# Kernel tuning notes

Hardware: AMD Instinct MI355X
Metric: run time of the kernel (lower is better)

## Reference

```python
import jax, jax.numpy as jnp
import numpy as np

K = 1024          # num_embeddings
D = 256           # embedding_dim
COMMIT = 0.25
DECAY = 0.99
EPS = 1e-05


def setup_inputs() -> dict:
    key = jax.random.key(0)
    k1, k2 = jax.random.split(key)
    inputs = jax.random.normal(k1, (16, 4096, D), dtype=jnp.float32)
    weight = jax.random.normal(k2, (K, D), dtype=jnp.float32) * 0.1
    ema_cluster_size = jnp.zeros((K,), dtype=jnp.float32)
    ema_embedding_avg = weight  # initialized as a clone of the weights
    return {
        "inputs": inputs,
        "weight": weight,
        "ema_cluster_size": ema_cluster_size,
        "ema_embedding_avg": ema_embedding_avg,
    }


def reference(inputs, weight, ema_cluster_size, ema_embedding_avg):
    B = inputs.shape[0]
    flat = inputs.reshape(-1, D)                      # [N, D]
    dist = (
        jnp.sum(flat * flat, axis=1, keepdims=True)
        + jnp.sum(weight * weight, axis=1)
        - 2.0 * (flat @ weight.T)
    )                                                 # [N, K]
    idx = jnp.argmin(dist, axis=1)                    # [N] int
    # one-hot @ weight == gather
    quantized = weight[idx].reshape(inputs.shape)

    # --- EMA codebook update (training-mode side effects, returned as outputs) ---
    counts = jax.ops.segment_sum(jnp.ones_like(idx, dtype=jnp.float32), idx, num_segments=K)
    emb_sum = jax.ops.segment_sum(flat, idx, num_segments=K)  # one_hot.T @ flat
    new_cluster_size = DECAY * ema_cluster_size + (1.0 - DECAY) * counts
    new_embedding_avg = DECAY * ema_embedding_avg + (1.0 - DECAY) * emb_sum
    n = jnp.sum(new_cluster_size)
    cs = (new_cluster_size + EPS) / (n + K * EPS) * n
    new_weight = new_embedding_avg / cs[:, None]

    # --- losses + straight-through estimator ---
    e_latent_loss = jnp.mean((jax.lax.stop_gradient(quantized) - inputs) ** 2)
    q_latent_loss = jnp.mean((quantized - jax.lax.stop_gradient(inputs)) ** 2)
    vq_loss = q_latent_loss + COMMIT * e_latent_loss
    quantized_st = inputs + jax.lax.stop_gradient(quantized - inputs)

    return (
        quantized_st,
        vq_loss,
        idx.reshape(B, -1),
        new_weight,
        new_cluster_size,
        new_embedding_avg,
    )
```

## Files before the change

kernel.cpp:

```cpp
#include <hip/hip_runtime.h>

#define KC 1024
#define DD 256
#define NROWS 65536
#define BM 128
#define NT 512
#define RESCUE_EPS 0.02f
#define RB 8

typedef _Float16 f16x8 __attribute__((ext_vector_type(8)));
typedef float f32x4 __attribute__((ext_vector_type(4)));
typedef const __attribute__((address_space(1))) unsigned int* gptr_t;
typedef __attribute__((address_space(3))) unsigned int* lptr_t;

__global__ void wprep(const float* __restrict__ W, _Float16* __restrict__ wh,
                      float* __restrict__ se) {
    int k = blockIdx.x, lane = threadIdx.x;
    float4 v = reinterpret_cast<const float4*>(W + (size_t)k * DD)[lane];
    float vv[4] = {v.x, v.y, v.z, v.w};
    _Float16 h4[4];
    double s = 0.0;
#pragma unroll
    for (int q = 0; q < 4; ++q) {
        h4[q] = (_Float16)vv[q];
        s += (double)vv[q] * vv[q];
    }
    *reinterpret_cast<uint2*>(wh + (size_t)k * DD + lane * 4) = *reinterpret_cast<uint2*>(h4);
    for (int m = 32; m >= 1; m >>= 1) s += __shfl_xor(s, m, 64);
    if (lane == 0) se[k] = (float)s;
}

__global__ __launch_bounds__(256) void wtrans4(const float* __restrict__ W,
                                               float4* __restrict__ WT4) {
    __shared__ __align__(16) float4 tile[64][65];
    const int c0 = blockIdx.x * 64;
    const int t = threadIdx.x;
    for (int it = 0; it < 16; ++it) {
        int idx = it * 256 + t;
        int cl = idx >> 6, d4 = idx & 63;
        tile[cl][d4] = reinterpret_cast<const float4*>(W + (size_t)(c0 + cl) * DD)[d4];
    }
    __syncthreads();
    for (int it = 0; it < 16; ++it) {
        int idx = it * 256 + t;
        int d4 = idx >> 6, cl = idx & 63;
        WT4[(size_t)d4 * KC + c0 + cl] = tile[cl][d4];
    }
}

__global__ __launch_bounds__(NT, 2) void vq_mfma(
    const float* __restrict__ X,
    const _Float16* __restrict__ wh,
    const float* __restrict__ se,
    float* __restrict__ out_q, float* __restrict__ out_idx,
    int* __restrict__ idx_int, float* __restrict__ sx_out,
    int* __restrict__ flags, int* __restrict__ count,
    float* __restrict__ counts, double* __restrict__ loss_acc)
{
    __shared__ __align__(16) _Float16 wt[2][64 * 256];
    __shared__ float sxs[BM];
    __shared__ float ses[KC];
    __shared__ int argidx[BM];
    __shared__ double lred[8];

    const int tid = threadIdx.x;
    const int row0 = blockIdx.x * BM;
    const int w = tid >> 6, lane = tid & 63;
    const int m = lane & 15, g = lane >> 4;

    for (int i = tid; i < KC; i += NT) ses[i] = se[i];

    f16x8 ahr[8];
    {
        const float* xr = X + (size_t)(row0 + w * 16 + m) * DD;
        float p0 = 0.f, p1 = 0.f, p2 = 0.f, p3 = 0.f;
#pragma unroll
        for (int ks = 0; ks < 8; ++ks) {
            float4 a = *reinterpret_cast<const float4*>(xr + ks * 32 + g * 8);
            float4 b = *reinterpret_cast<const float4*>(xr + ks * 32 + g * 8 + 4);
            float v[8] = {a.x, a.y, a.z, a.w, b.x, b.y, b.z, b.w};
            f16x8 h;
#pragma unroll
            for (int q = 0; q < 8; ++q) h[q] = (_Float16)v[q];
            ahr[ks] = h;
            p0 = fmaf(v[0], v[0], fmaf(v[4], v[4], p0));
            p1 = fmaf(v[1], v[1], fmaf(v[5], v[5], p1));
            p2 = fmaf(v[2], v[2], fmaf(v[6], v[6], p2));
            p3 = fmaf(v[3], v[3], fmaf(v[7], v[7], p3));
        }
        float ss = (p0 + p1) + (p2 + p3);
        ss += __shfl_xor(ss, 16, 64);
        ss += __shfl_xor(ss, 32, 64);
        if (g == 0) sxs[w * 16 + m] = ss;
    }

    auto stage = [&](int ct, int buf) {
        const int base = ct * 64;
#pragma unroll
        for (int p = 0; p < 4; ++p) {
            int gi = p * NT + tid;
            int code = gi >> 5, j = gi & 31;
            int kq = j ^ (code & 31);
            const _Float16* src = wh + (size_t)(base + code) * DD + kq * 8;
            __builtin_amdgcn_global_load_lds((gptr_t)(const void*)src,
                                             (lptr_t)(void*)&wt[buf][gi * 8], 16, 0, 0);
        }
    };

    stage(0, 0);
    __syncthreads();

    float b1[4], b2[4];
    int i1[4];
#pragma unroll
    for (int j = 0; j < 4; ++j) { b1[j] = 3.4e38f; b2[j] = 3.4e38f; i1[j] = 0; }

    float sxr[4];
#pragma unroll
    for (int j = 0; j < 4; ++j) sxr[j] = sxs[w * 16 + g * 4 + j];

    for (int ct = 0; ct < 16; ++ct) {
        const int buf = ct & 1;
        if (ct < 15) stage(ct + 1, buf ^ 1);

        const _Float16* wtb = wt[buf];
        f32x4 acc[4];
#pragma unroll
        for (int cs = 0; cs < 4; ++cs) acc[cs] = (f32x4){0.f, 0.f, 0.f, 0.f};

#pragma unroll
        for (int ks = 0; ks < 8; ++ks) {
            const int kq = ks * 4 + g;
#pragma unroll
            for (int cs = 0; cs < 4; ++cs) {
                const int code = cs * 16 + m;
                const int L = code * 32 + (kq ^ (code & 31));
                f16x8 bh = *reinterpret_cast<const f16x8*>(wtb + L * 8);
                acc[cs] = __builtin_amdgcn_mfma_f32_16x16x32_f16(ahr[ks], bh, acc[cs], 0, 0, 0);
            }
        }
#pragma unroll
        for (int cs = 0; cs < 4; ++cs) {
            const int code = ct * 64 + cs * 16 + m;
            const float sec = ses[code];
#pragma unroll
            for (int j = 0; j < 4; ++j) {
                float s = __fsub_rn(__fadd_rn(sxr[j], sec), __fmul_rn(2.0f, acc[cs][j]));
                if (s < b1[j]) { b2[j] = b1[j]; b1[j] = s; i1[j] = code; }
                else if (s < b2[j]) { b2[j] = s; }
            }
        }
        __syncthreads();
    }

#pragma unroll
    for (int j = 0; j < 4; ++j) {
        float v1 = b1[j], v2 = b2[j];
        int ix = i1[j];
        for (int mm = 1; mm < 16; mm <<= 1) {
            float ov1 = __shfl_xor(v1, mm, 64);
            int oi = __shfl_xor(ix, mm, 64);
            float ov2 = __shfl_xor(v2, mm, 64);
            float nv2 = fminf(fminf(v2, ov2), fmaxf(v1, ov1));
            if (ov1 < v1 || (ov1 == v1 && oi < ix)) { v1 = ov1; ix = oi; }
            v2 = nv2;
        }
        if (m == 0) {
            int rl = w * 16 + g * 4 + j;
            argidx[rl] = ix;
            if (v2 - v1 < RESCUE_EPS) {
                int p = atomicAdd(count, 1);
                flags[p] = row0 + rl;
            }
        }
    }
    __syncthreads();

    if (tid < BM) {
        int row = row0 + tid;
        int k = argidx[tid];
        idx_int[row] = k;
        out_idx[row] = (float)k;
        sx_out[row] = sxs[tid];
        atomicAdd(&counts[k], 1.0f);
    }

    {
        double lacc = 0.0;
        const int rl = w * 16 + m;
        const int row = row0 + rl;
        const int k = argidx[rl];
        const _Float16* qh = wh + (size_t)k * DD;
        float* orow = out_q + (size_t)row * DD;
#pragma unroll
        for (int ks = 0; ks < 8; ++ks) {
            const int col = ks * 32 + g * 8;
            union { uint4 u; _Float16 h[8]; } qv, xv;
            qv.u = *reinterpret_cast<const uint4*>(qh + col);
            xv.u = *reinterpret_cast<uint4*>(&ahr[ks]);
            float o8[8];
#pragma unroll
            for (int q = 0; q < 8; ++q) {
                float xf = (float)xv.h[q];
                float qf = (float)qv.h[q];
                float df = qf - xf;
                o8[q] = xf + df;
                lacc += (double)df * df;
            }
            *reinterpret_cast<float4*>(orow + col)     = *reinterpret_cast<float4*>(&o8[0]);
            *reinterpret_cast<float4*>(orow + col + 4) = *reinterpret_cast<float4*>(&o8[4]);
        }
        for (int mm = 32; mm >= 1; mm >>= 1) lacc += __shfl_xor(lacc, mm, 64);
        if (lane == 0) lred[w] = lacc;
    }
    __syncthreads();
    if (tid == 0) {
        double t = 0.0;
        for (int i = 0; i < 8; ++i) t += lred[i];
        atomicAdd(loss_acc, t);
    }
}

__global__ __launch_bounds__(256) void rescue(
    const float* __restrict__ X, const float4* __restrict__ WT4,
    const float* __restrict__ Wf,
    const float* __restrict__ se, const float* __restrict__ sx,
    const int* __restrict__ flags, const int* __restrict__ count,
    int* __restrict__ idx_int, float* __restrict__ out_idx,
    float* __restrict__ out_q, float* __restrict__ counts,
    double* __restrict__ loss_acc)
{
    __shared__ __align__(16) float xs[RB][DD];
    __shared__ float rv[RB][256];
    __shared__ int ri[RB][256];
    __shared__ float sxr_s[RB];
    __shared__ int rows_s[RB];
    __shared__ int kn_s[RB], ko_s[RB];
    __shared__ double dred[4];
    const int t = threadIdx.x;
    const int n = count[0];

    for (int base = blockIdx.x * RB; base < n; base += gridDim.x * RB) {
        const int nb = min(RB, n - base);
        for (int idx = t; idx < nb * 64; idx += 256) {
            int r = idx >> 6, c4 = idx & 63;
            float4 v = reinterpret_cast<const float4*>(X + (size_t)flags[base + r] * DD)[c4];
            *reinterpret_cast<float4*>(&xs[r][c4 * 4]) = v;
        }
        if (t < nb) { rows_s[t] = flags[base + t]; sxr_s[t] = sx[flags[base + t]]; }
        __syncthreads();

        float acc[4][RB];
#pragma unroll
        for (int cc = 0; cc < 4; ++cc)
#pragma unroll
            for (int r = 0; r < RB; ++r) acc[cc][r] = 0.0f;

        float4 wv[4], wn[4];
#pragma unroll
        for (int cc = 0; cc < 4; ++cc) wv[cc] = WT4[(size_t)0 * KC + cc * 256 + t];

        for (int d4 = 0; d4 < 64; ++d4) {
            const int dn = (d4 < 63) ? d4 + 1 : 63;
#pragma unroll
            for (int cc = 0; cc < 4; ++cc) wn[cc] = WT4[(size_t)dn * KC + cc * 256 + t];
#pragma unroll
            for (int r = 0; r < RB; ++r) {
                float4 xv = *reinterpret_cast<const float4*>(&xs[r][d4 * 4]);
#pragma unroll
                for (int cc = 0; cc < 4; ++cc)
                    acc[cc][r] = fmaf(xv.w, wv[cc].w, fmaf(xv.z, wv[cc].z,
                                 fmaf(xv.y, wv[cc].y, fmaf(xv.x, wv[cc].x, acc[cc][r]))));
            }
#pragma unroll
            for (int cc = 0; cc < 4; ++cc) wv[cc] = wn[cc];
        }

        float best[RB];
        int bidx[RB];
#pragma unroll
        for (int r = 0; r < RB; ++r) { best[r] = 3.4e38f; bidx[r] = 0; }
#pragma unroll
        for (int cc = 0; cc < 4; ++cc) {
            const int c = cc * 256 + t;
            const float sec = se[c];
#pragma unroll
            for (int r = 0; r < RB; ++r) {
                float s = __fsub_rn(__fadd_rn(sxr_s[r], sec), __fmul_rn(2.0f, acc[cc][r]));
                if (s < best[r] || (s == best[r] && c < bidx[r])) { best[r] = s; bidx[r] = c; }
            }
        }
#pragma unroll
        for (int r = 0; r < RB; ++r) { rv[r][t] = best[r]; ri[r][t] = bidx[r]; }
        __syncthreads();

        for (int sft = 128; sft >= 1; sft >>= 1) {
            if (t < sft) {
#pragma unroll
                for (int r = 0; r < RB; ++r) {
                    float ov = rv[r][t + sft];
                    int oi = ri[r][t + sft];
                    if (ov < rv[r][t] || (ov == rv[r][t] && oi < ri[r][t])) {
                        rv[r][t] = ov; ri[r][t] = oi;
                    }
                }
            }
            __syncthreads();
        }
        if (t < nb) {
            int row = rows_s[t];
            int kn = ri[t][0], ko = idx_int[row];
            kn_s[t] = kn; ko_s[t] = ko;
            if (kn != ko) {
                idx_int[row] = kn;
                out_idx[row] = (float)kn;
                atomicAdd(&counts[ko], -1.0f);
                atomicAdd(&counts[kn], 1.0f);
            }
        }
        __syncthreads();

        for (int r = 0; r < nb; ++r) {
            const int ko = ko_s[r], kn = kn_s[r];
            if (kn != ko) {
                const int row = rows_s[r];
                float x = xs[r][t];
                float qo = Wf[(size_t)ko * DD + t];
                float qn = Wf[(size_t)kn * DD + t];
                float dfn = qn - x, dfo = qo - x;
                out_q[(size_t)row * DD + t] = x + dfn;
                double dl = (double)dfn * dfn - (double)dfo * dfo;
                for (int mm = 32; mm >= 1; mm >>= 1) dl += __shfl_xor(dl, mm, 64);
                if ((t & 63) == 0) dred[t >> 6] = dl;
                __syncthreads();
                if (t == 0) atomicAdd(loss_acc, dred[0] + dred[1] + dred[2] + dred[3]);
                __syncthreads();
            }
        }
        __syncthreads();
    }
}

__global__ void prefix1024(const float* __restrict__ counts, int* __restrict__ off,
                           int* __restrict__ cur) {
    __shared__ int s[1024];
    int t = threadIdx.x;
    s[t] = (int)counts[t];
    __syncthreads();
    for (int d = 1; d < 1024; d <<= 1) {
        int v = (t >= d) ? s[t - d] : 0;
        __syncthreads();
        s[t] += v;
        __syncthreads();
    }
    off[t] = (t == 0) ? 0 : s[t - 1];
    cur[t] = 0;
    if (t == 0) off[1024] = 65536;
}

__global__ __launch_bounds__(256) void scatter_rows(
    const int* __restrict__ idx_int, const int* __restrict__ off,
    int* __restrict__ cur, int* __restrict__ sorted) {
    int i = blockIdx.x * 256 + threadIdx.x;
    int k = idx_int[i];
    int p = atomicAdd(&cur[k], 1);
    sorted[off[k] + p] = i;
}

__global__ __launch_bounds__(256) void emb_gather(
    const float* __restrict__ X, const int* __restrict__ off,
    const int* __restrict__ sorted, float* __restrict__ emb) {
    const int k = blockIdx.x, t = threadIdx.x;
    const int s0 = off[k], s1 = off[k + 1];
    float a0 = 0.f, a1 = 0.f, a2 = 0.f, a3 = 0.f;
    int i = s0;
    for (; i + 4 <= s1; i += 4) {
        int r0 = sorted[i], r1 = sorted[i + 1], r2 = sorted[i + 2], r3 = sorted[i + 3];
        a0 += X[(size_t)r0 * DD + t];
        a1 += X[(size_t)r1 * DD + t];
        a2 += X[(size_t)r2 * DD + t];
        a3 += X[(size_t)r3 * DD + t];
    }
    for (; i < s1; ++i) a0 += X[(size_t)sorted[i] * DD + t];
    emb[(size_t)k * DD + t] = (a0 + a1) + (a2 + a3);
}

__global__ void fin1(const float* __restrict__ ema_cs, float* __restrict__ ncs_buf,
                     const double* __restrict__ loss_acc, float* __restrict__ out_loss,
                     float* __restrict__ n_out)
{
    __shared__ float red[1024];
    int t = threadIdx.x;
    const float OM = (float)(1.0 - 0.99);
    float ncs = __fadd_rn(__fmul_rn(0.99f, ema_cs[t]), __fmul_rn(OM, ncs_buf[t]));
    ncs_buf[t] = ncs;
    red[t] = ncs;
    __syncthreads();
    for (int s = 512; s >= 1; s >>= 1) {
        if (t < s) red[t] += red[t + s];
        __syncthreads();
    }
    if (t == 0) {
        n_out[0] = red[0];
        float el = (float)(loss_acc[0] / 16777216.0);
        out_loss[0] = __fadd_rn(el, __fmul_rn(0.25f, el));
    }
}

__global__ __launch_bounds__(256) void fin2(const float* __restrict__ ema_avg,
                                            float* __restrict__ avg_buf,
                                            const float* __restrict__ ncs,
                                            const float* __restrict__ n_ptr,
                                            float* __restrict__ out_w)
{
    int k = blockIdx.x, d = threadIdx.x;
    const float OM = (float)(1.0 - 0.99);
    const float KEPS = (float)(1024.0 * 1e-5);
    size_t i = (size_t)k * DD + d;
    float avg = __fadd_rn(__fmul_rn(0.99f, ema_avg[i]), __fmul_rn(OM, avg_buf[i]));
    float n = n_ptr[0];
    float cs = __fmul_rn(__fdiv_rn(__fadd_rn(ncs[k], 1e-5f), __fadd_rn(n, KEPS)), n);
    avg_buf[i] = avg;
    out_w[i] = __fdiv_rn(avg, cs);
}

extern "C" void kernel_launch(void* const* d_in, const int* in_sizes, int n_in,
                              void* d_out, int out_size, void* d_ws, size_t ws_size,
                              hipStream_t stream) {
    const float* X = (const float*)d_in[0];
    const float* W = (const float*)d_in[1];
    const float* ema_cs = (const float*)d_in[2];
    const float* ema_avg = (const float*)d_in[3];

    float* out = (float*)d_out;
    float* out_q    = out;
    float* out_loss = out + 16777216;
    float* out_idx  = out + 16777217;
    float* out_w    = out + 16842753;
    float* out_ncs  = out + 17104897;
    float* out_avg  = out + 17105921;

    char* ws = (char*)d_ws;
    float* se      = (float*)(ws + 0);
    float* n_ptr   = (float*)(ws + 4096);
    double* loss   = (double*)(ws + 4112);
    int*   count   = (int*)(ws + 4128);
    _Float16* wh   = (_Float16*)(ws + 8192);
    float* sx      = (float*)(ws + 1056768);
    int*   idx_int = (int*)(ws + 1318912);
    int*   flags   = (int*)(ws + 1581056);
    float4* WT4    = (float4*)(ws + 2097152);
    int*   off     = (int*)(ws + 3145728);
    int*   cur     = (int*)(ws + 3153920);
    int*   sorted  = (int*)(ws + 3158016);

    hipMemsetAsync(out_ncs, 0, 1024 * sizeof(float), stream);
    hipMemsetAsync(loss, 0, sizeof(double), stream);
    hipMemsetAsync(count, 0, sizeof(int), stream);

    wprep<<<KC, 64, 0, stream>>>(W, wh, se);
    wtrans4<<<16, 256, 0, stream>>>(W, WT4);
    vq_mfma<<<NROWS / BM, NT, 0, stream>>>(X, wh, se, out_q, out_idx,
                                           idx_int, sx, flags, count,
                                           out_ncs, loss);
    rescue<<<512, 256, 0, stream>>>(X, WT4, W, se, sx, flags, count, idx_int, out_idx,
                                    out_q, out_ncs, loss);
    prefix1024<<<1, 1024, 0, stream>>>(out_ncs, off, cur);
    scatter_rows<<<NROWS / 256, 256, 0, stream>>>(idx_int, off, cur, sorted);
    emb_gather<<<KC, 256, 0, stream>>>(X, off, sorted, out_avg);
    fin1<<<1, 1024, 0, stream>>>(ema_cs, out_ncs, loss, out_loss, n_ptr);
    fin2<<<KC, 256, 0, stream>>>(ema_avg, out_avg, out_ncs, n_ptr, out_w);
}
```

Measured before the change: 188.9 us.

## Fuse auxiliary kernels and streamline conversions in VQ pipeline

Merges the codebook transpose into the weight-prep kernel, the prefix scan into the cluster-size finalizer, and the per-code embedding gather into the final EMA/weight kernel, removing three launches and an intermediate round trip through the embedding-average buffer. Uses packed round-toward-zero fp16 conversions, an fma distance expression, float loss accumulation and hoisted staging offsets in the main MFMA kernel. Rounding mode and precision of the loss and distances change slightly, and the fused transpose writes are strided.

```diff
diff --git a/kernel.cpp b/kernel.cpp
--- a/kernel.cpp
+++ b/kernel.cpp
@@ -9,43 +9,23 @@
 #define RB 8
 
 typedef _Float16 f16x8 __attribute__((ext_vector_type(8)));
+typedef __fp16 fp16x2 __attribute__((ext_vector_type(2)));
 typedef float f32x4 __attribute__((ext_vector_type(4)));
 typedef const __attribute__((address_space(1))) unsigned int* gptr_t;
 typedef __attribute__((address_space(3))) unsigned int* lptr_t;
 
 __global__ void wprep(const float* __restrict__ W, _Float16* __restrict__ wh,
-                      float* __restrict__ se) {
+                      float* __restrict__ se, float4* __restrict__ WT4) {
     int k = blockIdx.x, lane = threadIdx.x;
     float4 v = reinterpret_cast<const float4*>(W + (size_t)k * DD)[lane];
-    float vv[4] = {v.x, v.y, v.z, v.w};
-    _Float16 h4[4];
-    double s = 0.0;
-#pragma unroll
-    for (int q = 0; q < 4; ++q) {
-        h4[q] = (_Float16)vv[q];
-        s += (double)vv[q] * vv[q];
-    }
-    *reinterpret_cast<uint2*>(wh + (size_t)k * DD + lane * 4) = *reinterpret_cast<uint2*>(h4);
+    union { fp16x2 h2[2]; uint2 u; } cv;
+    cv.h2[0] = __builtin_amdgcn_cvt_pkrtz(v.x, v.y);
+    cv.h2[1] = __builtin_amdgcn_cvt_pkrtz(v.z, v.w);
+    *reinterpret_cast<uint2*>(wh + (size_t)k * DD + lane * 4) = cv.u;
+    WT4[(size_t)lane * KC + k] = v;
+    double s = (double)v.x * v.x + (double)v.y * v.y + (double)v.z * v.z + (double)v.w * v.w;
     for (int m = 32; m >= 1; m >>= 1) s += __shfl_xor(s, m, 64);
     if (lane == 0) se[k] = (float)s;
-}
-
-__global__ __launch_bounds__(256) void wtrans4(const float* __restrict__ W,
-                                               float4* __restrict__ WT4) {
-    __shared__ __align__(16) float4 tile[64][65];
-    const int c0 = blockIdx.x * 64;
-    const int t = threadIdx.x;
-    for (int it = 0; it < 16; ++it) {
-        int idx = it * 256 + t;
-        int cl = idx >> 6, d4 = idx & 63;
-        tile[cl][d4] = reinterpret_cast<const float4*>(W + (size_t)(c0 + cl) * DD)[d4];
-    }
-    __syncthreads();
-    for (int it = 0; it < 16; ++it) {
-        int idx = it * 256 + t;
-        int d4 = idx >> 6, cl = idx & 63;
-        WT4[(size_t)d4 * KC + c0 + cl] = tile[cl][d4];
-    }
 }
 
 __global__ __launch_bounds__(NT, 2) void vq_mfma(
@@ -78,15 +58,16 @@
         for (int ks = 0; ks < 8; ++ks) {
             float4 a = *reinterpret_cast<const float4*>(xr + ks * 32 + g * 8);
             float4 b = *reinterpret_cast<const float4*>(xr + ks * 32 + g * 8 + 4);
-            float v[8] = {a.x, a.y, a.z, a.w, b.x, b.y, b.z, b.w};
-            f16x8 h;
-#pragma unroll
-            for (int q = 0; q < 8; ++q) h[q] = (_Float16)v[q];
-            ahr[ks] = h;
-            p0 = fmaf(v[0], v[0], fmaf(v[4], v[4], p0));
-            p1 = fmaf(v[1], v[1], fmaf(v[5], v[5], p1));
-            p2 = fmaf(v[2], v[2], fmaf(v[6], v[6], p2));
-            p3 = fmaf(v[3], v[3], fmaf(v[7], v[7], p3));
+            union { fp16x2 h2[4]; f16x8 h8; } cv;
+            cv.h2[0] = __builtin_amdgcn_cvt_pkrtz(a.x, a.y);
+            cv.h2[1] = __builtin_amdgcn_cvt_pkrtz(a.z, a.w);
+            cv.h2[2] = __builtin_amdgcn_cvt_pkrtz(b.x, b.y);
+            cv.h2[3] = __builtin_amdgcn_cvt_pkrtz(b.z, b.w);
+            ahr[ks] = cv.h8;
+            p0 = fmaf(a.x, a.x, fmaf(b.x, b.x, p0));
+            p1 = fmaf(a.y, a.y, fmaf(b.y, b.y, p1));
+            p2 = fmaf(a.z, a.z, fmaf(b.z, b.z, p2));
+            p3 = fmaf(a.w, a.w, fmaf(b.w, b.w, p3));
         }
         float ss = (p0 + p1) + (p2 + p3);
         ss += __shfl_xor(ss, 16, 64);
@@ -94,17 +75,22 @@
         if (g == 0) sxs[w * 16 + m] = ss;
     }
 
+    size_t srcoff[4];
+    unsigned ldsoff[4];
+#pragma unroll
+    for (int p = 0; p < 4; ++p) {
+        int gi = p * NT + tid;
+        int code = gi >> 5, j = gi & 31;
+        int kq = j ^ (code & 31);
+        srcoff[p] = (size_t)code * DD + kq * 8;
+        ldsoff[p] = gi * 8;
+    }
     auto stage = [&](int ct, int buf) {
-        const int base = ct * 64;
-#pragma unroll
-        for (int p = 0; p < 4; ++p) {
-            int gi = p * NT + tid;
-            int code = gi >> 5, j = gi & 31;
-            int kq = j ^ (code & 31);
-            const _Float16* src = wh + (size_t)(base + code) * DD + kq * 8;
-            __builtin_amdgcn_global_load_lds((gptr_t)(const void*)src,
-                                             (lptr_t)(void*)&wt[buf][gi * 8], 16, 0, 0);
-        }
+        const _Float16* b = wh + (size_t)ct * 64 * DD;
+#pragma unroll
+        for (int p = 0; p < 4; ++p)
+            __builtin_amdgcn_global_load_lds((gptr_t)(const void*)(b + srcoff[p]),
+                                             (lptr_t)(void*)&wt[buf][ldsoff[p]], 16, 0, 0);
     };
 
     stage(0, 0);
@@ -145,7 +131,7 @@
             const float sec = ses[code];
 #pragma unroll
             for (int j = 0; j < 4; ++j) {
-                float s = __fsub_rn(__fadd_rn(sxr[j], sec), __fmul_rn(2.0f, acc[cs][j]));
+                float s = fmaf(-2.0f, acc[cs][j], sxr[j] + sec);
                 if (s < b1[j]) { b2[j] = b1[j]; b1[j] = s; i1[j] = code; }
                 else if (s < b2[j]) { b2[j] = s; }
             }
@@ -186,7 +172,7 @@
     }
 
     {
-        double lacc = 0.0;
+        float lacc = 0.0f;
         const int rl = w * 16 + m;
         const int row = row0 + rl;
         const int k = argidx[rl];
@@ -201,17 +187,16 @@
             float o8[8];
 #pragma unroll
             for (int q = 0; q < 8; ++q) {
-                float xf = (float)xv.h[q];
                 float qf = (float)qv.h[q];
-                float df = qf - xf;
-                o8[q] = xf + df;
-                lacc += (double)df * df;
+                float df = qf - (float)xv.h[q];
+                o8[q] = qf;
+                lacc = fmaf(df, df, lacc);
             }
             *reinterpret_cast<float4*>(orow + col)     = *reinterpret_cast<float4*>(&o8[0]);
             *reinterpret_cast<float4*>(orow + col + 4) = *reinterpret_cast<float4*>(&o8[4]);
         }
         for (int mm = 32; mm >= 1; mm >>= 1) lacc += __shfl_xor(lacc, mm, 64);
-        if (lane == 0) lred[w] = lacc;
+        if (lane == 0) lred[w] = (double)lacc;
     }
     __syncthreads();
     if (tid == 0) {
@@ -341,12 +326,30 @@
     }
 }
 
-__global__ void prefix1024(const float* __restrict__ counts, int* __restrict__ off,
-                           int* __restrict__ cur) {
+__global__ void finprefix(const float* __restrict__ ema_cs, float* __restrict__ ncs_buf,
+                          const double* __restrict__ loss_acc, float* __restrict__ out_loss,
+                          float* __restrict__ n_out, int* __restrict__ off,
+                          int* __restrict__ cur)
+{
+    __shared__ float red[1024];
     __shared__ int s[1024];
     int t = threadIdx.x;
-    s[t] = (int)counts[t];
+    const float OM = (float)(1.0 - 0.99);
+    float cnt = ncs_buf[t];
+    s[t] = (int)cnt;
+    float ncs = __fadd_rn(__fmul_rn(0.99f, ema_cs[t]), __fmul_rn(OM, cnt));
+    ncs_buf[t] = ncs;
+    red[t] = ncs;
     __syncthreads();
+    for (int st = 512; st >= 1; st >>= 1) {
+        if (t < st) red[t] += red[t + st];
+        __syncthreads();
+    }
+    if (t == 0) {
+        n_out[0] = red[0];
+        float el = (float)(loss_acc[0] / 16777216.0);
+        out_loss[0] = __fadd_rn(el, __fmul_rn(0.25f, el));
+    }
     for (int d = 1; d < 1024; d <<= 1) {
         int v = (t >= d) ? s[t - d] : 0;
         __syncthreads();
@@ -355,7 +358,7 @@
     }
     off[t] = (t == 0) ? 0 : s[t - 1];
     cur[t] = 0;
-    if (t == 0) off[1024] = 65536;
+    if (t == 0) off[1024] = NROWS;
 }
 
 __global__ __launch_bounds__(256) void scatter_rows(
@@ -367,9 +370,12 @@
     sorted[off[k] + p] = i;
 }
 
-__global__ __launch_bounds__(256) void emb_gather(
+__global__ __launch_bounds__(256) void embfin2(
     const float* __restrict__ X, const int* __restrict__ off,
-    const int* __restrict__ sorted, float* __restrict__ emb) {
+    const int* __restrict__ sorted, const float* __restrict__ ema_avg,
+    const float* __restrict__ ncs, const float* __restrict__ n_ptr,
+    float* __restrict__ out_avg, float* __restrict__ out_w)
+{
     const int k = blockIdx.x, t = threadIdx.x;
     const int s0 = off[k], s1 = off[k + 1];
     float a0 = 0.f, a1 = 0.f, a2 = 0.f, a3 = 0.f;
@@ -382,46 +388,16 @@
         a3 += X[(size_t)r3 * DD + t];
     }
     for (; i < s1; ++i) a0 += X[(size_t)sorted[i] * DD + t];
-    emb[(size_t)k * DD + t] = (a0 + a1) + (a2 + a3);
-}
-
-__global__ void fin1(const float* __restrict__ ema_cs, float* __restrict__ ncs_buf,
-                     const double* __restrict__ loss_acc, float* __restrict__ out_loss,
-                     float* __restrict__ n_out)
-{
-    __shared__ float red[1024];
-    int t = threadIdx.x;
-    const float OM = (float)(1.0 - 0.99);
-    float ncs = __fadd_rn(__fmul_rn(0.99f, ema_cs[t]), __fmul_rn(OM, ncs_buf[t]));
-    ncs_buf[t] = ncs;
-    red[t] = ncs;
-    __syncthreads();
-    for (int s = 512; s >= 1; s >>= 1) {
-        if (t < s) red[t] += red[t + s];
-        __syncthreads();
-    }
-    if (t == 0) {
-        n_out[0] = red[0];
-        float el = (float)(loss_acc[0] / 16777216.0);
-        out_loss[0] = __fadd_rn(el, __fmul_rn(0.25f, el));
-    }
-}
-
-__global__ __launch_bounds__(256) void fin2(const float* __restrict__ ema_avg,
-                                            float* __restrict__ avg_buf,
-                                            const float* __restrict__ ncs,
-                                            const float* __restrict__ n_ptr,
-                                            float* __restrict__ out_w)
-{
-    int k = blockIdx.x, d = threadIdx.x;
+    float total = (a0 + a1) + (a2 + a3);
+
     const float OM = (float)(1.0 - 0.99);
     const float KEPS = (float)(1024.0 * 1e-5);
-    size_t i = (size_t)k * DD + d;
-    float avg = __fadd_rn(__fmul_rn(0.99f, ema_avg[i]), __fmul_rn(OM, avg_buf[i]));
+    size_t o = (size_t)k * DD + t;
+    float avg = __fadd_rn(__fmul_rn(0.99f, ema_avg[o]), __fmul_rn(OM, total));
     float n = n_ptr[0];
     float cs = __fmul_rn(__fdiv_rn(__fadd_rn(ncs[k], 1e-5f), __fadd_rn(n, KEPS)), n);
-    avg_buf[i] = avg;
-    out_w[i] = __fdiv_rn(avg, cs);
+    out_avg[o] = avg;
+    out_w[o] = __fdiv_rn(avg, cs);
 }
 
 extern "C" void kernel_launch(void* const* d_in, const int* in_sizes, int n_in,
@@ -458,16 +434,14 @@
     hipMemsetAsync(loss, 0, sizeof(double), stream);
     hipMemsetAsync(count, 0, sizeof(int), stream);
 
-    wprep<<<KC, 64, 0, stream>>>(W, wh, se);
-    wtrans4<<<16, 256, 0, stream>>>(W, WT4);
+    wprep<<<KC, 64, 0, stream>>>(W, wh, se, WT4);
     vq_mfma<<<NROWS / BM, NT, 0, stream>>>(X, wh, se, out_q, out_idx,
                                            idx_int, sx, flags, count,
                                            out_ncs, loss);
     rescue<<<512, 256, 0, stream>>>(X, WT4, W, se, sx, flags, count, idx_int, out_idx,
                                     out_q, out_ncs, loss);
-    prefix1024<<<1, 1024, 0, stream>>>(out_ncs, off, cur);
+    finprefix<<<1, 1024, 0, stream>>>(ema_cs, out_ncs, loss, out_loss, n_ptr, off, cur);
     scatter_rows<<<NROWS / 256, 256, 0, stream>>>(idx_int, off, cur, sorted);
-    emb_gather<<<KC, 256, 0, stream>>>(X, off, sorted, out_avg);
-    fin1<<<1, 1024, 0, stream>>>(ema_cs, out_ncs, loss, out_loss, n_ptr);
-    fin2<<<KC, 256, 0, stream>>>(ema_avg, out_avg, out_ncs, n_ptr, out_w);
-}
+    embfin2<<<KC, 256, 0, stream>>>(X, off, sorted, ema_avg, out_ncs, n_ptr,
+                                    out_avg, out_w);
+}
```

New measurement: 183.7 us. 1.03x faster.
